# Kernel optimization log

Measured on AMD Instinct MI355X. Metric: run time of the kernel, lower is better.

Reference implementation:

```python
import jax, jax.numpy as jnp
import numpy as np

N = 50000      # nodes
E = 800000     # edges (before self loops)
G = 64         # graphs in batch
F_IN = 11
HID = 64
C = 8
NEG_SLOPE = 0.2


def setup_inputs() -> dict:
    key = jax.random.key(0)
    ks = jax.random.split(key, 20)
    inp = {
        "x": jax.random.normal(ks[0], (N, F_IN), dtype=jnp.float32),
        "edge_index": jax.random.randint(ks[1], (2, E), 0, N, dtype=jnp.int64),
        "edge_attr": jax.random.normal(ks[2], (E, 17), dtype=jnp.float32),
        "batch": jnp.sort(jax.random.randint(ks[3], (N,), 0, G, dtype=jnp.int64)),
    }
    def glorot(k, shape):
        fan_in, fan_out = shape[0], shape[-1]
        s = jnp.sqrt(6.0 / (fan_in + fan_out))
        return jax.random.uniform(k, shape, jnp.float32, -s, s)
    # GATConv layers (heads=1): W [in,out], att vectors a_src/a_dst [out], bias [out]
    inp["W1"] = glorot(ks[4], (F_IN, HID)); inp["a1s"] = glorot(ks[5], (HID,)); inp["a1d"] = glorot(ks[6], (HID,)); inp["b1"] = jnp.zeros((HID,), jnp.float32)
    inp["W2"] = glorot(ks[7], (HID, HID)); inp["a2s"] = glorot(ks[8], (HID,)); inp["a2d"] = glorot(ks[9], (HID,)); inp["b2"] = jnp.zeros((HID,), jnp.float32)
    inp["W3"] = glorot(ks[10], (HID, C)); inp["a3s"] = glorot(ks[11], (C,)); inp["a3d"] = glorot(ks[12], (C,)); inp["b3"] = jnp.zeros((C,), jnp.float32)
    return inp


def _gat_layer(x, src, dst, W, a_s, a_d, b):
    # x: [N,in] -> h: [N,out]; single head, concat irrelevant for heads=1
    h = x @ W
    alpha_src = h @ a_s            # [N]
    alpha_dst = h @ a_d            # [N]
    e = jax.nn.leaky_relu(alpha_src[src] + alpha_dst[dst], negative_slope=NEG_SLOPE)  # [E']
    # segment-wise (per destination node) softmax over incoming edges
    m = jax.ops.segment_max(e, dst, num_segments=N)
    ex = jnp.exp(e - m[dst])
    denom = jax.ops.segment_sum(ex, dst, num_segments=N)
    alpha = ex / denom[dst]
    out = jax.ops.segment_sum(alpha[:, None] * h[src], dst, num_segments=N)
    return out + b


def reference(x, edge_index, edge_attr, batch, W1, a1s, a1d, b1, W2, a2s, a2d, b2, W3, a3s, a3d, b3):
    del edge_attr  # GATConv without edge_dim ignores edge_attr
    loop = jnp.arange(N, dtype=edge_index.dtype)
    src = jnp.concatenate([edge_index[0], loop])  # add self loops
    dst = jnp.concatenate([edge_index[1], loop])
    h = jax.nn.relu(_gat_layer(x, src, dst, W1, a1s, a1d, b1))
    h = jax.nn.relu(_gat_layer(h, src, dst, W2, a2s, a2d, b2))
    h = jax.nn.relu(_gat_layer(h, src, dst, W3, a3s, a3d, b3))
    # global mean pool over graphs
    counts = jax.ops.segment_sum(jnp.ones((N,), h.dtype), batch, num_segments=G)
    pooled = jax.ops.segment_sum(h, batch, num_segments=G) / jnp.maximum(counts, 1.0)[:, None]
    # dropout is identity in eval mode
    return jax.nn.sigmoid(pooled)
```

## Files before the change

### kernel.cpp

```cpp
#include <hip/hip_runtime.h>
#include <hip/hip_bf16.h>

#define NN 50000
#define EE 800000
#define GG 64
#define CC 8

#define NBKT 196
#define CHUNK 4096
#define NCHK 196
#define CAP 8192

__device__ __forceinline__ float lrelu(float z) { return fmaxf(z, 0.2f * z); }


__global__ __launch_bounds__(256) void kA1(const int* __restrict__ dst, int* __restrict__ G) {
    __shared__ int hist[NBKT];
    int t = threadIdx.x;
    for (int i = t; i < NBKT; i += 256) hist[i] = 0;
    __syncthreads();
    int e0 = blockIdx.x * CHUNK;
    int e1 = min(e0 + CHUNK, EE);
    for (int e = e0 + t; e < e1; e += 256) atomicAdd(&hist[dst[e] >> 8], 1);
    __syncthreads();
    for (int i = t; i < NBKT; i += 256) G[blockIdx.x * NBKT + i] = hist[i];
}

__global__ __launch_bounds__(256) void kA2(const int* __restrict__ G, int* __restrict__ offs,
                                           int* __restrict__ bT) {
    __shared__ int s[256];
    int t = threadIdx.x, j = blockIdx.x;
    int v = (t < NCHK) ? G[t * NBKT + j] : 0;
    s[t] = v;
    __syncthreads();
#pragma unroll
    for (int off = 1; off < 256; off <<= 1) {
        int u = (t >= off) ? s[t - off] : 0;
        __syncthreads();
        s[t] += u;
        __syncthreads();
    }
    if (t < NCHK) offs[t * NBKT + j] = s[t] - v;
    if (t == 255) bT[j] = s[255];
}

__global__ __launch_bounds__(256) void kA2b(const int* __restrict__ bT, int* __restrict__ bstart,
                                            float* __restrict__ pool, float* __restrict__ cntf,
                                            int* __restrict__ rowptr) {
    __shared__ int s[256];
    int t = threadIdx.x;
    int v = (t < NBKT) ? bT[t] : 0;
    s[t] = v;
    __syncthreads();
#pragma unroll
    for (int off = 1; off < 256; off <<= 1) {
        int u = (t >= off) ? s[t - off] : 0;
        __syncthreads();
        s[t] += u;
        __syncthreads();
    }
    if (t < NBKT) bstart[t] = s[t] - v;
    if (t == 0) { bstart[NBKT] = EE; rowptr[NN] = EE; }
    for (int i = t; i < GG * CC; i += 256) pool[i] = 0.f;
    if (t < GG) cntf[t] = 0.f;
}

__global__ __launch_bounds__(256) void kA3(const int* __restrict__ src, const int* __restrict__ dst,
                                           const int* __restrict__ offs, const int* __restrict__ bstart,
                                           uint2* __restrict__ pairs) {
    __shared__ int cur[NBKT];
    int t = threadIdx.x, c = blockIdx.x;
    for (int i = t; i < NBKT; i += 256) cur[i] = bstart[i] + offs[c * NBKT + i];
    __syncthreads();
    int e0 = c * CHUNK, e1 = min(e0 + CHUNK, EE);
    for (int e = e0 + t; e < e1; e += 256) {
        int d = dst[e];
        int pos = atomicAdd(&cur[d >> 8], 1);
        pairs[pos] = make_uint2((unsigned)src[e], (unsigned)d);
    }
}

__global__ __launch_bounds__(256) void kB(const uint2* __restrict__ pairs, const int* __restrict__ bstart,
                                          int* __restrict__ col, int* __restrict__ rowptr) {
    __shared__ int srcL[CAP];
    __shared__ unsigned short dstL[CAP];
    __shared__ int hist[256];
    __shared__ int sc[256];
    int t = threadIdx.x, j = blockIdx.x;
    int start = bstart[j], end = bstart[j + 1];
    int cnt = end - start;
    if (cnt > CAP) cnt = CAP;
    int nb = j * 256;
    int nodeCnt = min(256, NN - nb);
    hist[t] = 0;
    __syncthreads();
    for (int i = t; i < cnt; i += 256) {
        uint2 p = pairs[start + i];
        srcL[i] = (int)p.x;
        int dl = (int)p.y - nb;
        dstL[i] = (unsigned short)dl;
        atomicAdd(&hist[dl], 1);
    }
    __syncthreads();
    int c = hist[t];
    sc[t] = c;
    __syncthreads();
#pragma unroll
    for (int off = 1; off < 256; off <<= 1) {
        int u = (t >= off) ? sc[t - off] : 0;
        __syncthreads();
        sc[t] += u;
        __syncthreads();
    }
    int excl = sc[t] - c;
    if (t < nodeCnt) rowptr[nb + t] = start + excl;
    hist[t] = excl;
    __syncthreads();
    for (int i = t; i < cnt; i += 256) {
        int dl = dstL[i];
        int pos = atomicAdd(&hist[dl], 1);
        col[start + pos] = srcL[i];
    }
}


template <int IN>
__global__ __launch_bounds__(256) void k_mm64t(const float* __restrict__ x, const float* __restrict__ W,
                                               const float* __restrict__ avs, const float* __restrict__ avd,
                                               float* __restrict__ h, float* __restrict__ as_,
                                               float* __restrict__ ad_) {
    __shared__ float xT[IN * 68];
    __shared__ float Wl[IN * 64];
    __shared__ float avl[64], adl[64];
    int t = threadIdx.x;
    int nbase = blockIdx.x * 64;
    for (int idx = t; idx < IN * 64; idx += 256) Wl[idx] = W[idx];
    if (t < 64) { avl[t] = avs[t]; adl[t] = avd[t]; }
    for (int idx = t; idx < 64 * IN; idx += 256) {
        int n = idx / IN, k = idx - n * IN;
        int gn = nbase + n;
        if (gn >= NN) gn = NN - 1;
        xT[k * 68 + n] = x[gn * IN + k];
    }
    __syncthreads();
    int f0 = (t & 15) * 4;
    int n0 = (t >> 4) * 4;
    float a00=0,a01=0,a02=0,a03=0, a10=0,a11=0,a12=0,a13=0;
    float a20=0,a21=0,a22=0,a23=0, a30=0,a31=0,a32=0,a33=0;
#pragma unroll 4
    for (int k = 0; k < IN; k++) {
        float4 xv = *(const float4*)&xT[k * 68 + n0];
        float4 wv = *(const float4*)&Wl[k * 64 + f0];
        a00 += xv.x * wv.x; a01 += xv.x * wv.y; a02 += xv.x * wv.z; a03 += xv.x * wv.w;
        a10 += xv.y * wv.x; a11 += xv.y * wv.y; a12 += xv.y * wv.z; a13 += xv.y * wv.w;
        a20 += xv.z * wv.x; a21 += xv.z * wv.y; a22 += xv.z * wv.z; a23 += xv.z * wv.w;
        a30 += xv.w * wv.x; a31 += xv.w * wv.y; a32 += xv.w * wv.z; a33 += xv.w * wv.w;
    }
    float4 av = *(const float4*)&avl[f0];
    float4 dv = *(const float4*)&adl[f0];
    float vs[4], vd[4];
    vs[0] = a00*av.x + a01*av.y + a02*av.z + a03*av.w;
    vs[1] = a10*av.x + a11*av.y + a12*av.z + a13*av.w;
    vs[2] = a20*av.x + a21*av.y + a22*av.z + a23*av.w;
    vs[3] = a30*av.x + a31*av.y + a32*av.z + a33*av.w;
    vd[0] = a00*dv.x + a01*dv.y + a02*dv.z + a03*dv.w;
    vd[1] = a10*dv.x + a11*dv.y + a12*dv.z + a13*dv.w;
    vd[2] = a20*dv.x + a21*dv.y + a22*dv.z + a23*dv.w;
    vd[3] = a30*dv.x + a31*dv.y + a32*dv.z + a33*dv.w;
#pragma unroll
    for (int o = 1; o < 16; o <<= 1) {
#pragma unroll
        for (int ni = 0; ni < 4; ni++) {
            vs[ni] += __shfl_xor(vs[ni], o);
            vd[ni] += __shfl_xor(vd[ni], o);
        }
    }
    float4* h4 = (float4*)h;
    int nn0 = nbase + n0;
    if (nn0 + 3 < NN) {
        h4[(nn0 + 0) * 16 + (t & 15)] = make_float4(a00, a01, a02, a03);
        h4[(nn0 + 1) * 16 + (t & 15)] = make_float4(a10, a11, a12, a13);
        h4[(nn0 + 2) * 16 + (t & 15)] = make_float4(a20, a21, a22, a23);
        h4[(nn0 + 3) * 16 + (t & 15)] = make_float4(a30, a31, a32, a33);
        if ((t & 15) == 0) {
#pragma unroll
            for (int ni = 0; ni < 4; ni++) { as_[nn0 + ni] = vs[ni]; ad_[nn0 + ni] = vd[ni]; }
        }
    } else {
        float rows[4][4] = {{a00,a01,a02,a03},{a10,a11,a12,a13},{a20,a21,a22,a23},{a30,a31,a32,a33}};
#pragma unroll
        for (int ni = 0; ni < 4; ni++) {
            if (nn0 + ni < NN) {
                h4[(nn0 + ni) * 16 + (t & 15)] = make_float4(rows[ni][0], rows[ni][1], rows[ni][2], rows[ni][3]);
                if ((t & 15) == 0) { as_[nn0 + ni] = vs[ni]; ad_[nn0 + ni] = vd[ni]; }
            }
        }
    }
}

__global__ __launch_bounds__(256) void k_mm8(const float* __restrict__ x, const float* __restrict__ W,
                                             const float* __restrict__ avs, const float* __restrict__ avd,
                                             float* __restrict__ h3, float* __restrict__ as_,
                                             float* __restrict__ ad_) {
    __shared__ float Wl[512];
    for (int idx = threadIdx.x; idx < 512; idx += 256) Wl[idx] = W[idx];
    __syncthreads();
    int node = blockIdx.x * 4 + (threadIdx.x >> 6);
    int lane = threadIdx.x & 63;
    if (node >= NN) return;
    int f = lane & 7, kc = lane >> 3;
    float xv = x[node * 64 + lane];
    float acc = 0.f;
#pragma unroll
    for (int j = 0; j < 8; j++) {
        int k = kc * 8 + j;
        acc += __shfl(xv, k) * Wl[k * 8 + f];
    }
    acc += __shfl_xor(acc, 8);
    acc += __shfl_xor(acc, 16);
    acc += __shfl_xor(acc, 32);
    if (lane < 8) h3[node * 8 + lane] = acc;
    float vs = 0.f, vd = 0.f;
    if (lane < 8) {
        vs = acc * avs[lane];
        vd = acc * avd[lane];
    }
    vs += __shfl_xor(vs, 1); vs += __shfl_xor(vs, 2); vs += __shfl_xor(vs, 4);
    vd += __shfl_xor(vd, 1); vd += __shfl_xor(vd, 2); vd += __shfl_xor(vd, 4);
    if (lane == 0) {
        as_[node] = vs;
        ad_[node] = vd;
    }
}


__global__ __launch_bounds__(256) void k_agg64(const float* __restrict__ h, const int* __restrict__ rowptr,
                                               const int* __restrict__ col, const float* __restrict__ as_,
                                               const float* __restrict__ ad_, const float* __restrict__ bias,
                                               float* __restrict__ out) {
    int node = blockIdx.x * 4 + (threadIdx.x >> 6);
    int lane = threadIdx.x & 63;
    if (node >= NN) return;
    int rp0 = rowptr[node];
    int deg = rowptr[node + 1] - rp0;
    float adn = ad_[node];
    float zself = lrelu(as_[node] + adn);
    const float4* h4 = (const float4*)h;
    int f = lane & 15, eg = lane >> 4;
    float4 acc = make_float4(0.f, 0.f, 0.f, 0.f);
    if (deg <= 64) {
        int s = 0;
        float z = -1e30f;
        if (lane < deg) {
            s = col[rp0 + lane];
            z = lrelu(as_[s] + adn);
        }
        float M = z;
#pragma unroll
        for (int o = 32; o; o >>= 1) M = fmaxf(M, __shfl_xor(M, o));
        M = fmaxf(M, zself);
        float ex = (lane < deg) ? __expf(z - M) : 0.f;
        float exs = __expf(zself - M);
        float sum = ex;
#pragma unroll
        for (int o = 32; o; o >>= 1) sum += __shfl_xor(sum, o);
        float inv = 1.f / (sum + exs);
        float wl = ex * inv;
        int base = 0;
        for (; base + 8 <= deg; base += 8) {
            int ia = base + eg, ib = base + 4 + eg;
            int sa = __shfl(s, ia), sb = __shfl(s, ib);
            float wa = __shfl(wl, ia), wb = __shfl(wl, ib);
            float4 ha = h4[sa * 16 + f];
            float4 hb = h4[sb * 16 + f];
            acc.x += wa * ha.x + wb * hb.x;
            acc.y += wa * ha.y + wb * hb.y;
            acc.z += wa * ha.z + wb * hb.z;
            acc.w += wa * ha.w + wb * hb.w;
        }
        for (; base < deg; base += 4) {
            int ia = base + eg;
            int sa = __shfl(s, ia);
            float wa = __shfl(wl, ia);
            float4 ha = h4[sa * 16 + f];
            acc.x += wa * ha.x;
            acc.y += wa * ha.y;
            acc.z += wa * ha.z;
            acc.w += wa * ha.w;
        }
        if (eg == 0) {
            float w0 = exs * inv;
            float4 hv = h4[node * 16 + f];
            acc.x += w0 * hv.x;
            acc.y += w0 * hv.y;
            acc.z += w0 * hv.z;
            acc.w += w0 * hv.w;
        }
    } else {
        float m = -1e30f, l = 0.f;
        for (int i = lane; i < deg; i += 64) {
            float z = lrelu(as_[col[rp0 + i]] + adn);
            float mn = fmaxf(m, z);
            l = l * __expf(m - mn) + __expf(z - mn);
            m = mn;
        }
        if (lane == 0) {
            float mn = fmaxf(m, zself);
            l = l * __expf(m - mn) + __expf(zself - mn);
            m = mn;
        }
#pragma unroll
        for (int o = 32; o; o >>= 1) {
            float mo = __shfl_xor(m, o), lo = __shfl_xor(l, o);
            float mn = fmaxf(m, mo);
            l = l * __expf(m - mn) + lo * __expf(mo - mn);
            m = mn;
        }
        float Em = m;
        float inv = 1.f / l;
        for (int base = 0; base < deg; base += 4) {
            int i = base + eg;
            if (i < deg) {
                int sv = col[rp0 + i];
                float al = __expf(lrelu(as_[sv] + adn) - Em) * inv;
                float4 hv = h4[sv * 16 + f];
                acc.x += al * hv.x;
                acc.y += al * hv.y;
                acc.z += al * hv.z;
                acc.w += al * hv.w;
            }
        }
        if (eg == 0) {
            float al = __expf(zself - Em) * inv;
            float4 hv = h4[node * 16 + f];
            acc.x += al * hv.x;
            acc.y += al * hv.y;
            acc.z += al * hv.z;
            acc.w += al * hv.w;
        }
    }
#pragma unroll
    for (int o = 16; o <= 32; o <<= 1) {
        acc.x += __shfl_xor(acc.x, o);
        acc.y += __shfl_xor(acc.y, o);
        acc.z += __shfl_xor(acc.z, o);
        acc.w += __shfl_xor(acc.w, o);
    }
    if (eg == 0) {
        float4 bv = ((const float4*)bias)[f];
        float4 o4;
        o4.x = fmaxf(acc.x + bv.x, 0.f);
        o4.y = fmaxf(acc.y + bv.y, 0.f);
        o4.z = fmaxf(acc.z + bv.z, 0.f);
        o4.w = fmaxf(acc.w + bv.w, 0.f);
        ((float4*)out)[node * 16 + f] = o4;
    }
}

__global__ __launch_bounds__(256) void k_agg8(const float* __restrict__ h, const int* __restrict__ rowptr,
                                              const int* __restrict__ col, const float* __restrict__ as_,
                                              const float* __restrict__ ad_, const float* __restrict__ bias,
                                              float* __restrict__ out) {
    int node = blockIdx.x * 4 + (threadIdx.x >> 6);
    int lane = threadIdx.x & 63;
    if (node >= NN) return;
    int rp0 = rowptr[node];
    int deg = rowptr[node + 1] - rp0;
    float adn = ad_[node];
    float zself = lrelu(as_[node] + adn);
    const float2* h2v = (const float2*)h;
    int f = lane & 3, eg = lane >> 2;
    float2 acc = make_float2(0.f, 0.f);
    if (deg <= 64) {
        int s = 0;
        float z = -1e30f;
        if (lane < deg) {
            s = col[rp0 + lane];
            z = lrelu(as_[s] + adn);
        }
        float M = z;
#pragma unroll
        for (int o = 32; o; o >>= 1) M = fmaxf(M, __shfl_xor(M, o));
        M = fmaxf(M, zself);
        float ex = (lane < deg) ? __expf(z - M) : 0.f;
        float exs = __expf(zself - M);
        float sum = ex;
#pragma unroll
        for (int o = 32; o; o >>= 1) sum += __shfl_xor(sum, o);
        float inv = 1.f / (sum + exs);
        float wl = ex * inv;
        for (int base = 0; base < deg; base += 16) {
            int ia = base + eg;
            int sa = __shfl(s, ia);
            float wa = __shfl(wl, ia);
            float2 hv = h2v[sa * 4 + f];
            acc.x += wa * hv.x;
            acc.y += wa * hv.y;
        }
        if (eg == 0) {
            float w0 = exs * inv;
            float2 hv = h2v[node * 4 + f];
            acc.x += w0 * hv.x;
            acc.y += w0 * hv.y;
        }
    } else {
        float m = -1e30f, l = 0.f;
        for (int i = lane; i < deg; i += 64) {
            float z = lrelu(as_[col[rp0 + i]] + adn);
            float mn = fmaxf(m, z);
            l = l * __expf(m - mn) + __expf(z - mn);
            m = mn;
        }
        if (lane == 0) {
            float mn = fmaxf(m, zself);
            l = l * __expf(m - mn) + __expf(zself - mn);
            m = mn;
        }
#pragma unroll
        for (int o = 32; o; o >>= 1) {
            float mo = __shfl_xor(m, o), lo = __shfl_xor(l, o);
            float mn = fmaxf(m, mo);
            l = l * __expf(m - mn) + lo * __expf(mo - mn);
            m = mn;
        }
        float Em = m;
        float inv = 1.f / l;
        for (int base = 0; base < deg; base += 16) {
            int i = base + eg;
            if (i < deg) {
                int sv = col[rp0 + i];
                float al = __expf(lrelu(as_[sv] + adn) - Em) * inv;
                float2 hv = h2v[sv * 4 + f];
                acc.x += al * hv.x;
                acc.y += al * hv.y;
            }
        }
        if (eg == 0) {
            float al = __expf(zself - Em) * inv;
            float2 hv = h2v[node * 4 + f];
            acc.x += al * hv.x;
            acc.y += al * hv.y;
        }
    }
#pragma unroll
    for (int o = 4; o <= 32; o <<= 1) {
        acc.x += __shfl_xor(acc.x, o);
        acc.y += __shfl_xor(acc.y, o);
    }
    if (eg == 0) {
        float2 bv = ((const float2*)bias)[f];
        float2 o2;
        o2.x = fmaxf(acc.x + bv.x, 0.f);
        o2.y = fmaxf(acc.y + bv.y, 0.f);
        ((float2*)out)[node * 4 + f] = o2;
    }
}


__global__ __launch_bounds__(256) void k_pool(const float* __restrict__ h3, const int* __restrict__ batch,
                                              float* __restrict__ pool, float* __restrict__ cntf) {
    __shared__ float pl[GG * CC + GG];
    for (int idx = threadIdx.x; idx < GG * CC + GG; idx += 256) pl[idx] = 0.f;
    __syncthreads();
    int node = blockIdx.x * 256 + threadIdx.x;
    if (node < NN) {
        int g = batch[node];
#pragma unroll
        for (int c = 0; c < CC; c++) atomicAdd(&pl[g * CC + c], h3[node * CC + c]);
        atomicAdd(&pl[GG * CC + g], 1.0f);
    }
    __syncthreads();
    for (int idx = threadIdx.x; idx < GG * CC + GG; idx += 256) {
        float v = pl[idx];
        if (idx < GG * CC)
            atomicAdd(&pool[idx], v);
        else
            atomicAdd(&cntf[idx - GG * CC], v);
    }
}

__global__ void k_final(const float* __restrict__ pool, const float* __restrict__ cntf,
                        float* __restrict__ out) {
    int t = threadIdx.x;
    if (t < GG * CC) {
        int g = t >> 3;
        float c = fmaxf(cntf[g], 1.0f);
        float v = pool[t] / c;
        out[t] = 1.0f / (1.0f + __expf(-v));
    }
}


extern "C" void kernel_launch(void* const* d_in, const int* in_sizes, int n_in,
                              void* d_out, int out_size, void* d_ws, size_t ws_size,
                              hipStream_t stream) {
    const float* x   = (const float*)d_in[0];
    const int*   ei  = (const int*)d_in[1];
    const int*   bat = (const int*)d_in[3];
    const float* W1  = (const float*)d_in[4];
    const float* a1s = (const float*)d_in[5];
    const float* a1d = (const float*)d_in[6];
    const float* b1  = (const float*)d_in[7];
    const float* W2  = (const float*)d_in[8];
    const float* a2s = (const float*)d_in[9];
    const float* a2d = (const float*)d_in[10];
    const float* b2  = (const float*)d_in[11];
    const float* W3  = (const float*)d_in[12];
    const float* a3s = (const float*)d_in[13];
    const float* a3d = (const float*)d_in[14];
    const float* b3  = (const float*)d_in[15];
    float* out = (float*)d_out;

    float* hA  = (float*)d_ws;
    float* hB  = hA + NN * 64;
    float* h3a = hB + NN * 64;
    float* h3b = h3a + NN * 8;
    float* as_ = h3b + NN * 8;
    float* ad_ = as_ + NN;
    int* rowptr  = (int*)(ad_ + NN);
    int* col     = rowptr + NN + 1;
    int* G       = col + EE;
    int* offs    = G + NCHK * NBKT;
    int* bT      = offs + NCHK * NBKT;
    int* bstart  = bT + NBKT;
    float* pool  = (float*)(bstart + NBKT + 1);
    float* cntf  = pool + GG * CC;
    uint2* pairs = (uint2*)hA;

    const int NB4  = (NN + 3) / 4;
    const int NB64 = (NN + 63) / 64;
    const int NBN  = (NN + 255) / 256;

    const int* srcE = ei;
    const int* dstE = ei + EE;

    kA1<<<NCHK, 256, 0, stream>>>(dstE, G);
    kA2<<<NBKT, 256, 0, stream>>>(G, offs, bT);
    kA2b<<<1, 256, 0, stream>>>(bT, bstart, pool, cntf, rowptr);
    kA3<<<NCHK, 256, 0, stream>>>(srcE, dstE, offs, bstart, pairs);
    kB<<<NBKT, 256, 0, stream>>>(pairs, bstart, col, rowptr);

    k_mm64t<11><<<NB64, 256, 0, stream>>>(x, W1, a1s, a1d, hA, as_, ad_);
    k_agg64<<<NB4, 256, 0, stream>>>(hA, rowptr, col, as_, ad_, b1, hB);
    k_mm64t<64><<<NB64, 256, 0, stream>>>(hB, W2, a2s, a2d, hA, as_, ad_);
    k_agg64<<<NB4, 256, 0, stream>>>(hA, rowptr, col, as_, ad_, b2, hB);
    k_mm8<<<NB4, 256, 0, stream>>>(hB, W3, a3s, a3d, h3a, as_, ad_);
    k_agg8<<<NB4, 256, 0, stream>>>(h3a, rowptr, col, as_, ad_, b3, h3b);
    k_pool<<<NBN, 256, 0, stream>>>(h3b, bat, pool, cntf);
    k_final<<<1, 512, 0, stream>>>(pool, cntf, out);
}
```

Baseline: 307.2 us.

## Store node features in bf16 and pack edge pairs into 32-bit words

Projected node features h are now written as bf16 by the matmul kernels and read back as bf16 in the aggregation kernels, halving the bytes of the random neighbor gathers. The CSR build packs each edge's source index (16 bits) and local destination (8 bits) into one 32-bit word instead of a uint2, halving traffic in the bucket scatter and in kB. The aggregation kernels also stage the per-edge weight and source index in shared memory and read them as uint4, replacing per-edge shuffles. Storing features in bf16 adds rounding error. Packing the source into 16 bits truncates indices at or above 65536, which is safe here only because N is 50000.

```diff
diff --git a/kernel.cpp b/kernel.cpp
--- a/kernel.cpp
+++ b/kernel.cpp
@@ -12,6 +12,14 @@
 #define CAP 8192
 
 __device__ __forceinline__ float lrelu(float z) { return fmaxf(z, 0.2f * z); }
+
+__device__ __forceinline__ unsigned short f2bf(float v) {
+    unsigned u = __float_as_uint(v);
+    return (unsigned short)((u + 0x7FFFu + ((u >> 16) & 1u)) >> 16);
+}
+__device__ __forceinline__ float bf2f(unsigned short b) {
+    return __uint_as_float(((unsigned)b) << 16);
+}
 
 
 __global__ __launch_bounds__(256) void kA1(const int* __restrict__ dst, int* __restrict__ G) {
@@ -67,7 +75,7 @@
 
 __global__ __launch_bounds__(256) void kA3(const int* __restrict__ src, const int* __restrict__ dst,
                                            const int* __restrict__ offs, const int* __restrict__ bstart,
-                                           uint2* __restrict__ pairs) {
+                                           unsigned* __restrict__ pairs) {
     __shared__ int cur[NBKT];
     int t = threadIdx.x, c = blockIdx.x;
     for (int i = t; i < NBKT; i += 256) cur[i] = bstart[i] + offs[c * NBKT + i];
@@ -76,14 +84,13 @@
     for (int e = e0 + t; e < e1; e += 256) {
         int d = dst[e];
         int pos = atomicAdd(&cur[d >> 8], 1);
-        pairs[pos] = make_uint2((unsigned)src[e], (unsigned)d);
-    }
-}
-
-__global__ __launch_bounds__(256) void kB(const uint2* __restrict__ pairs, const int* __restrict__ bstart,
+        pairs[pos] = (unsigned)src[e] | ((unsigned)(d & 255) << 16);
+    }
+}
+
+__global__ __launch_bounds__(256) void kB(const unsigned* __restrict__ pairs, const int* __restrict__ bstart,
                                           int* __restrict__ col, int* __restrict__ rowptr) {
-    __shared__ int srcL[CAP];
-    __shared__ unsigned short dstL[CAP];
+    __shared__ unsigned pL[CAP];
     __shared__ int hist[256];
     __shared__ int sc[256];
     int t = threadIdx.x, j = blockIdx.x;
@@ -95,11 +102,9 @@
     hist[t] = 0;
     __syncthreads();
     for (int i = t; i < cnt; i += 256) {
-        uint2 p = pairs[start + i];
-        srcL[i] = (int)p.x;
-        int dl = (int)p.y - nb;
-        dstL[i] = (unsigned short)dl;
-        atomicAdd(&hist[dl], 1);
+        unsigned p = pairs[start + i];
+        pL[i] = p;
+        atomicAdd(&hist[p >> 16], 1);
     }
     __syncthreads();
     int c = hist[t];
@@ -117,9 +122,9 @@
     hist[t] = excl;
     __syncthreads();
     for (int i = t; i < cnt; i += 256) {
-        int dl = dstL[i];
-        int pos = atomicAdd(&hist[dl], 1);
-        col[start + pos] = srcL[i];
+        unsigned p = pL[i];
+        int pos = atomicAdd(&hist[p >> 16], 1);
+        col[start + pos] = (int)(p & 0xFFFFu);
     }
 }
 
@@ -127,7 +132,7 @@
 template <int IN>
 __global__ __launch_bounds__(256) void k_mm64t(const float* __restrict__ x, const float* __restrict__ W,
                                                const float* __restrict__ avs, const float* __restrict__ avd,
-                                               float* __restrict__ h, float* __restrict__ as_,
+                                               unsigned short* __restrict__ h, float* __restrict__ as_,
                                                float* __restrict__ ad_) {
     __shared__ float xT[IN * 68];
     __shared__ float Wl[IN * 64];
@@ -175,32 +180,24 @@
             vd[ni] += __shfl_xor(vd[ni], o);
         }
     }
-    float4* h4 = (float4*)h;
+    ushort4* h4 = (ushort4*)h;
     int nn0 = nbase + n0;
-    if (nn0 + 3 < NN) {
-        h4[(nn0 + 0) * 16 + (t & 15)] = make_float4(a00, a01, a02, a03);
-        h4[(nn0 + 1) * 16 + (t & 15)] = make_float4(a10, a11, a12, a13);
-        h4[(nn0 + 2) * 16 + (t & 15)] = make_float4(a20, a21, a22, a23);
-        h4[(nn0 + 3) * 16 + (t & 15)] = make_float4(a30, a31, a32, a33);
-        if ((t & 15) == 0) {
-#pragma unroll
-            for (int ni = 0; ni < 4; ni++) { as_[nn0 + ni] = vs[ni]; ad_[nn0 + ni] = vd[ni]; }
-        }
-    } else {
-        float rows[4][4] = {{a00,a01,a02,a03},{a10,a11,a12,a13},{a20,a21,a22,a23},{a30,a31,a32,a33}};
-#pragma unroll
-        for (int ni = 0; ni < 4; ni++) {
-            if (nn0 + ni < NN) {
-                h4[(nn0 + ni) * 16 + (t & 15)] = make_float4(rows[ni][0], rows[ni][1], rows[ni][2], rows[ni][3]);
-                if ((t & 15) == 0) { as_[nn0 + ni] = vs[ni]; ad_[nn0 + ni] = vd[ni]; }
-            }
+    float rows[4][4] = {{a00,a01,a02,a03},{a10,a11,a12,a13},{a20,a21,a22,a23},{a30,a31,a32,a33}};
+#pragma unroll
+    for (int ni = 0; ni < 4; ni++) {
+        if (nn0 + ni < NN) {
+            ushort4 pv;
+            pv.x = f2bf(rows[ni][0]); pv.y = f2bf(rows[ni][1]);
+            pv.z = f2bf(rows[ni][2]); pv.w = f2bf(rows[ni][3]);
+            h4[(nn0 + ni) * 16 + (t & 15)] = pv;
+            if ((t & 15) == 0) { as_[nn0 + ni] = vs[ni]; ad_[nn0 + ni] = vd[ni]; }
         }
     }
 }
 
 __global__ __launch_bounds__(256) void k_mm8(const float* __restrict__ x, const float* __restrict__ W,
                                              const float* __restrict__ avs, const float* __restrict__ avd,
-                                             float* __restrict__ h3, float* __restrict__ as_,
+                                             unsigned short* __restrict__ h3, float* __restrict__ as_,
                                              float* __restrict__ ad_) {
     __shared__ float Wl[512];
     for (int idx = threadIdx.x; idx < 512; idx += 256) Wl[idx] = W[idx];
@@ -219,7 +216,7 @@
     acc += __shfl_xor(acc, 8);
     acc += __shfl_xor(acc, 16);
     acc += __shfl_xor(acc, 32);
-    if (lane < 8) h3[node * 8 + lane] = acc;
+    if (lane < 8) h3[node * 8 + lane] = f2bf(acc);
     float vs = 0.f, vd = 0.f;
     if (lane < 8) {
         vs = acc * avs[lane];
@@ -234,18 +231,20 @@
 }
 
 
-__global__ __launch_bounds__(256) void k_agg64(const float* __restrict__ h, const int* __restrict__ rowptr,
+__global__ __launch_bounds__(256) void k_agg64(const unsigned short* __restrict__ h,
+                                               const int* __restrict__ rowptr,
                                                const int* __restrict__ col, const float* __restrict__ as_,
                                                const float* __restrict__ ad_, const float* __restrict__ bias,
                                                float* __restrict__ out) {
-    int node = blockIdx.x * 4 + (threadIdx.x >> 6);
+    __shared__ uint2 ws[4][64];
+    int wid = threadIdx.x >> 6;
+    int node = blockIdx.x * 4 + wid;
     int lane = threadIdx.x & 63;
-    if (node >= NN) return;
     int rp0 = rowptr[node];
     int deg = rowptr[node + 1] - rp0;
     float adn = ad_[node];
     float zself = lrelu(as_[node] + adn);
-    const float4* h4 = (const float4*)h;
+    const ushort4* hb = (const ushort4*)h;
     int f = lane & 15, eg = lane >> 4;
     float4 acc = make_float4(0.f, 0.f, 0.f, 0.f);
     if (deg <= 64) {
@@ -266,37 +265,30 @@
         for (int o = 32; o; o >>= 1) sum += __shfl_xor(sum, o);
         float inv = 1.f / (sum + exs);
         float wl = ex * inv;
-        int base = 0;
-        for (; base + 8 <= deg; base += 8) {
-            int ia = base + eg, ib = base + 4 + eg;
-            int sa = __shfl(s, ia), sb = __shfl(s, ib);
-            float wa = __shfl(wl, ia), wb = __shfl(wl, ib);
-            float4 ha = h4[sa * 16 + f];
-            float4 hb = h4[sb * 16 + f];
-            acc.x += wa * ha.x + wb * hb.x;
-            acc.y += wa * ha.y + wb * hb.y;
-            acc.z += wa * ha.z + wb * hb.z;
-            acc.w += wa * ha.w + wb * hb.w;
-        }
-        for (; base < deg; base += 4) {
-            int ia = base + eg;
-            int sa = __shfl(s, ia);
-            float wa = __shfl(wl, ia);
-            float4 ha = h4[sa * 16 + f];
-            acc.x += wa * ha.x;
-            acc.y += wa * ha.y;
-            acc.z += wa * ha.z;
-            acc.w += wa * ha.w;
+        ws[wid][lane] = make_uint2(__float_as_uint(wl), (unsigned)s);
+        __syncthreads();
+        const uint4* wsp = (const uint4*)&ws[wid][0];
+        for (int base = 0; base < deg; base += 8) {
+            uint4 p = wsp[(base >> 1) + eg];
+            float wa = __uint_as_float(p.x);
+            float wb = __uint_as_float(p.z);
+            ushort4 ha = hb[p.y * 16 + f];
+            ushort4 hc = hb[p.w * 16 + f];
+            acc.x += wa * bf2f(ha.x) + wb * bf2f(hc.x);
+            acc.y += wa * bf2f(ha.y) + wb * bf2f(hc.y);
+            acc.z += wa * bf2f(ha.z) + wb * bf2f(hc.z);
+            acc.w += wa * bf2f(ha.w) + wb * bf2f(hc.w);
         }
         if (eg == 0) {
             float w0 = exs * inv;
-            float4 hv = h4[node * 16 + f];
-            acc.x += w0 * hv.x;
-            acc.y += w0 * hv.y;
-            acc.z += w0 * hv.z;
-            acc.w += w0 * hv.w;
+            ushort4 hv = hb[node * 16 + f];
+            acc.x += w0 * bf2f(hv.x);
+            acc.y += w0 * bf2f(hv.y);
+            acc.z += w0 * bf2f(hv.z);
+            acc.w += w0 * bf2f(hv.w);
         }
     } else {
+        __syncthreads();
         float m = -1e30f, l = 0.f;
         for (int i = lane; i < deg; i += 64) {
             float z = lrelu(as_[col[rp0 + i]] + adn);
@@ -323,20 +315,20 @@
             if (i < deg) {
                 int sv = col[rp0 + i];
                 float al = __expf(lrelu(as_[sv] + adn) - Em) * inv;
-                float4 hv = h4[sv * 16 + f];
-                acc.x += al * hv.x;
-                acc.y += al * hv.y;
-                acc.z += al * hv.z;
-                acc.w += al * hv.w;
+                ushort4 hv = hb[sv * 16 + f];
+                acc.x += al * bf2f(hv.x);
+                acc.y += al * bf2f(hv.y);
+                acc.z += al * bf2f(hv.z);
+                acc.w += al * bf2f(hv.w);
             }
         }
         if (eg == 0) {
             float al = __expf(zself - Em) * inv;
-            float4 hv = h4[node * 16 + f];
-            acc.x += al * hv.x;
-            acc.y += al * hv.y;
-            acc.z += al * hv.z;
-            acc.w += al * hv.w;
+            ushort4 hv = hb[node * 16 + f];
+            acc.x += al * bf2f(hv.x);
+            acc.y += al * bf2f(hv.y);
+            acc.z += al * bf2f(hv.z);
+            acc.w += al * bf2f(hv.w);
         }
     }
 #pragma unroll
@@ -357,18 +349,20 @@
     }
 }
 
-__global__ __launch_bounds__(256) void k_agg8(const float* __restrict__ h, const int* __restrict__ rowptr,
+__global__ __launch_bounds__(256) void k_agg8(const unsigned short* __restrict__ h,
+                                              const int* __restrict__ rowptr,
                                               const int* __restrict__ col, const float* __restrict__ as_,
                                               const float* __restrict__ ad_, const float* __restrict__ bias,
                                               float* __restrict__ out) {
-    int node = blockIdx.x * 4 + (threadIdx.x >> 6);
+    __shared__ uint2 ws[4][64];
+    int wid = threadIdx.x >> 6;
+    int node = blockIdx.x * 4 + wid;
     int lane = threadIdx.x & 63;
-    if (node >= NN) return;
     int rp0 = rowptr[node];
     int deg = rowptr[node + 1] - rp0;
     float adn = ad_[node];
     float zself = lrelu(as_[node] + adn);
-    const float2* h2v = (const float2*)h;
+    const ushort2* h2v = (const ushort2*)h;
     int f = lane & 3, eg = lane >> 2;
     float2 acc = make_float2(0.f, 0.f);
     if (deg <= 64) {
@@ -389,21 +383,26 @@
         for (int o = 32; o; o >>= 1) sum += __shfl_xor(sum, o);
         float inv = 1.f / (sum + exs);
         float wl = ex * inv;
-        for (int base = 0; base < deg; base += 16) {
-            int ia = base + eg;
-            int sa = __shfl(s, ia);
-            float wa = __shfl(wl, ia);
-            float2 hv = h2v[sa * 4 + f];
-            acc.x += wa * hv.x;
-            acc.y += wa * hv.y;
+        ws[wid][lane] = make_uint2(__float_as_uint(wl), (unsigned)s);
+        __syncthreads();
+        const uint4* wsp = (const uint4*)&ws[wid][0];
+        for (int base = 0; base < deg; base += 32) {
+            uint4 p = wsp[(base >> 1) + eg];
+            float wa = __uint_as_float(p.x);
+            float wb = __uint_as_float(p.z);
+            ushort2 ha = h2v[p.y * 4 + f];
+            ushort2 hc = h2v[p.w * 4 + f];
+            acc.x += wa * bf2f(ha.x) + wb * bf2f(hc.x);
+            acc.y += wa * bf2f(ha.y) + wb * bf2f(hc.y);
         }
         if (eg == 0) {
             float w0 = exs * inv;
-            float2 hv = h2v[node * 4 + f];
-            acc.x += w0 * hv.x;
-            acc.y += w0 * hv.y;
+            ushort2 hv = h2v[node * 4 + f];
+            acc.x += w0 * bf2f(hv.x);
+            acc.y += w0 * bf2f(hv.y);
         }
     } else {
+        __syncthreads();
         float m = -1e30f, l = 0.f;
         for (int i = lane; i < deg; i += 64) {
             float z = lrelu(as_[col[rp0 + i]] + adn);
@@ -430,16 +429,16 @@
             if (i < deg) {
                 int sv = col[rp0 + i];
                 float al = __expf(lrelu(as_[sv] + adn) - Em) * inv;
-                float2 hv = h2v[sv * 4 + f];
-                acc.x += al * hv.x;
-                acc.y += al * hv.y;
+                ushort2 hv = h2v[sv * 4 + f];
+                acc.x += al * bf2f(hv.x);
+                acc.y += al * bf2f(hv.y);
             }
         }
         if (eg == 0) {
             float al = __expf(zself - Em) * inv;
-            float2 hv = h2v[node * 4 + f];
-            acc.x += al * hv.x;
-            acc.y += al * hv.y;
+            ushort2 hv = h2v[node * 4 + f];
+            acc.x += al * bf2f(hv.x);
+            acc.y += al * bf2f(hv.y);
         }
     }
 #pragma unroll
@@ -525,7 +524,10 @@
     int* bstart  = bT + NBKT;
     float* pool  = (float*)(bstart + NBKT + 1);
     float* cntf  = pool + GG * CC;
-    uint2* pairs = (uint2*)hA;
+    unsigned* pairs = (unsigned*)hA;
+
+    unsigned short* hA16 = (unsigned short*)hA;
+    unsigned short* h316 = (unsigned short*)h3a;
 
     const int NB4  = (NN + 3) / 4;
     const int NB64 = (NN + 63) / 64;
@@ -540,12 +542,12 @@
     kA3<<<NCHK, 256, 0, stream>>>(srcE, dstE, offs, bstart, pairs);
     kB<<<NBKT, 256, 0, stream>>>(pairs, bstart, col, rowptr);
 
-    k_mm64t<11><<<NB64, 256, 0, stream>>>(x, W1, a1s, a1d, hA, as_, ad_);
-    k_agg64<<<NB4, 256, 0, stream>>>(hA, rowptr, col, as_, ad_, b1, hB);
-    k_mm64t<64><<<NB64, 256, 0, stream>>>(hB, W2, a2s, a2d, hA, as_, ad_);
-    k_agg64<<<NB4, 256, 0, stream>>>(hA, rowptr, col, as_, ad_, b2, hB);
-    k_mm8<<<NB4, 256, 0, stream>>>(hB, W3, a3s, a3d, h3a, as_, ad_);
-    k_agg8<<<NB4, 256, 0, stream>>>(h3a, rowptr, col, as_, ad_, b3, h3b);
+    k_mm64t<11><<<NB64, 256, 0, stream>>>(x, W1, a1s, a1d, hA16, as_, ad_);
+    k_agg64<<<NB4, 256, 0, stream>>>(hA16, rowptr, col, as_, ad_, b1, hB);
+    k_mm64t<64><<<NB64, 256, 0, stream>>>(hB, W2, a2s, a2d, hA16, as_, ad_);
+    k_agg64<<<NB4, 256, 0, stream>>>(hA16, rowptr, col, as_, ad_, b2, hB);
+    k_mm8<<<NB4, 256, 0, stream>>>(hB, W3, a3s, a3d, h316, as_, ad_);
+    k_agg8<<<NB4, 256, 0, stream>>>(h316, rowptr, col, as_, ad_, b3, h3b);
     k_pool<<<NBN, 256, 0, stream>>>(h3b, bat, pool, cntf);
     k_final<<<1, 512, 0, stream>>>(pool, cntf, out);
 }
```

New measurement: 283.6 us. 7.7% less time.
